# Kernel tuning notes

Measured on AMD Instinct MI355X. Metric: run time of the kernel, lower is better.

The kernel has to match this reference:

```python
import jax, jax.numpy as jnp
import numpy as np

HIDDEN = 768
N_HEADS = 12
HEAD_DIM = HIDDEN // N_HEADS  # 64 (multihead=True)
NEG_BIG = -1e31


def setup_inputs() -> dict:
    key = jax.random.key(0)
    ks = jax.random.split(key, 8)
    B, S = 4, 2048
    toks = jax.random.normal(ks[0], (B, S, HIDDEN), dtype=jnp.float32)
    masks = jax.random.randint(ks[1], (B, S), 0, 2, dtype=jnp.int32)
    s = 0.02
    Wq = jax.random.normal(ks[2], (HIDDEN, HIDDEN), dtype=jnp.float32) * s
    Wk = jax.random.normal(ks[3], (HIDDEN, HIDDEN), dtype=jnp.float32) * s
    Wv = jax.random.normal(ks[4], (HIDDEN, HIDDEN), dtype=jnp.float32) * s
    bq = jax.random.normal(ks[5], (HIDDEN,), dtype=jnp.float32) * s
    bk = jax.random.normal(ks[6], (HIDDEN,), dtype=jnp.float32) * s
    bv = jax.random.normal(ks[7], (HIDDEN,), dtype=jnp.float32) * s
    return {"toks": toks, "masks": masks, "Wq": Wq, "bq": bq,
            "Wk": Wk, "bk": bk, "Wv": Wv, "bv": bv}


def reference(toks, masks, Wq, bq, Wk, bk, Wv, bv):
    B, S, D = toks.shape
    m = masks.astype(jnp.float32)  # [B,S]
    # additive outer-product padding mask: (1 - m_i*m_j) * -1e31, shape [B,S,S]
    add_mask = (1.0 - m[:, :, None] * m[:, None, :]) * NEG_BIG

    def split_heads(x):  # [B,S,D] -> [B,H,S,hd]
        return x.reshape(B, S, N_HEADS, HEAD_DIM).transpose(0, 2, 1, 3)

    q = split_heads(toks @ Wq + bq)
    k = split_heads(toks @ Wk + bk)
    v = split_heads(toks @ Wv + bv)

    scores = jnp.einsum("bhqd,bhkd->bhqk", q, k) / jnp.sqrt(
        jnp.asarray(HEAD_DIM, dtype=toks.dtype))
    scores = scores + add_mask[:, None, :, :]
    probs = jax.nn.softmax(scores, axis=-1)  # dropout is identity at eval
    ctx = jnp.einsum("bhqk,bhkd->bhqd", probs, v)
    return ctx.transpose(0, 2, 1, 3).reshape(B, S, D)
```

## Files before the change

kernel.cpp:

```cpp
#include <hip/hip_runtime.h>
#include <hip/hip_bf16.h>
#include <cstddef>


typedef __bf16 bf16_8 __attribute__((ext_vector_type(8)));
typedef float f32x4 __attribute__((ext_vector_type(4)));
typedef short s16x4 __attribute__((ext_vector_type(4)));
typedef short s16x8 __attribute__((ext_vector_type(8)));

#define HID 768
#define NHEADS 12
#define HD 64
#define BATCH 4
#define SEQ 2048
#define NEGBIG2 (-1.44269504e31f)
#define SCALE2 0.18033688f

#define KT 64
#define NKT (SEQ / KT)
#define STR 68
#define ASTR 40

static __device__ __forceinline__ f32x4 mfma16x16x32(bf16_8 a, bf16_8 b, f32x4 c) {
  return __builtin_amdgcn_mfma_f32_16x16x32_bf16(a, b, c, 0, 0, 0);
}

static __device__ __forceinline__ void lds_barrier() {
  __asm__ volatile("s_waitcnt lgkmcnt(0)\n\ts_barrier" ::: "memory");
}

static __device__ __forceinline__ float fast_exp2(float x) {
#if __has_builtin(__builtin_amdgcn_exp2f)
  return __builtin_amdgcn_exp2f(x);
#else
  return __expf(x * 0.69314718f);
#endif
}

static __device__ __forceinline__ s16x4 pack_bf16x4(f32x4 p) {
  s16x4 o;
#pragma unroll
  for (int i = 0; i < 4; ++i) {
    __bf16 b = (__bf16)p[i];
    o[i] = __builtin_bit_cast(short, b);
  }
  return o;
}

static __device__ __forceinline__ bf16_8 cat2(const __bf16* p) {
  s16x4 lo = *(const s16x4*)p;
  s16x4 hi = *(const s16x4*)(p + 4);
  s16x8 v = __builtin_shufflevector(lo, hi, 0, 1, 2, 3, 4, 5, 6, 7);
  return __builtin_bit_cast(bf16_8, v);
}

static __device__ __forceinline__ void write2(__bf16* p, s16x8 v) {
  *(s16x4*)p = __builtin_shufflevector(v, v, 0, 1, 2, 3);
  *(s16x4*)(p + 4) = __builtin_shufflevector(v, v, 4, 5, 6, 7);
}

static __device__ __forceinline__ bf16_8 cvt_a_frag(const float* p) {
  f32x4 af0 = *(const f32x4*)p;
  f32x4 af1 = *(const f32x4*)(p + 4);
  bf16_8 a;
  a[0] = (__bf16)af0[0]; a[1] = (__bf16)af0[1];
  a[2] = (__bf16)af0[2]; a[3] = (__bf16)af0[3];
  a[4] = (__bf16)af1[0]; a[5] = (__bf16)af1[1];
  a[6] = (__bf16)af1[2]; a[7] = (__bf16)af1[3];
  return a;
}

__global__ __launch_bounds__(256) void mask_kadd(const int* __restrict__ masks,
                                                 float* __restrict__ kaddG) {
  int i = blockIdx.x * 256 + threadIdx.x;
  kaddG[i] = masks[i] ? 0.0f : NEGBIG2;
}

__global__ __launch_bounds__(256) void transpose768x3(const float* __restrict__ Wq,
                                                      const float* __restrict__ Wk,
                                                      const float* __restrict__ Wv,
                                                      __bf16* __restrict__ WtBase) {
  const float* in = blockIdx.z == 0 ? Wq : (blockIdx.z == 1 ? Wk : Wv);
  __bf16* out = WtBase + (size_t)blockIdx.z * HID * HID;
  __shared__ __bf16 tile[32][33];
  int bx = blockIdx.x * 32, by = blockIdx.y * 32;
  int tx = threadIdx.x, ty = threadIdx.y;
#pragma unroll
  for (int r = 0; r < 32; r += 8)
    tile[ty + r][tx] = (__bf16)in[(size_t)(by + ty + r) * HID + bx + tx];
  __syncthreads();
#pragma unroll
  for (int r = 0; r < 32; r += 8)
    out[(size_t)(bx + ty + r) * HID + by + tx] = tile[tx][ty + r];
}

__global__ __launch_bounds__(256, 4) void proj_kv(const float* __restrict__ toks,
                                                  const __bf16* __restrict__ WtK,
                                                  const float* __restrict__ bk,
                                                  const __bf16* __restrict__ WtV,
                                                  const float* __restrict__ bv,
                                                  __bf16* __restrict__ Kout,
                                                  __bf16* __restrict__ Vtout,
                                                  int head0, int hm) {
  __shared__ __align__(16) __bf16 ldsA[2][64 * ASTR];
  int tid = threadIdx.x;
  int w = tid >> 6, lane = tid & 63, l16 = lane & 15, quad = lane >> 4;
  int m0 = blockIdx.x * 64;
  int hl = blockIdx.y, h = head0 + hl;
  int srow = tid >> 2, scg = tid & 3;
  const float* asrc = toks + (size_t)(m0 + srow) * HID + scg * 8;
  const __bf16* bKrow = WtK + (size_t)(h * 64 + w * 16 + l16) * HID + quad * 8;
  const __bf16* bVrow = WtV + (size_t)(h * 64 + w * 16 + l16) * HID + quad * 8;
  f32x4 zero = {0.f, 0.f, 0.f, 0.f};
  f32x4 aK[4], aV[4];
#pragma unroll
  for (int mt = 0; mt < 4; ++mt) { aK[mt] = zero; aV[mt] = zero; }

  *(bf16_8*)(&ldsA[0][srow * ASTR + scg * 8]) = cvt_a_frag(asrc);
  __syncthreads();

  const int NCH = HID / 32;
  for (int t = 0; t < NCH; ++t) {
    int b = t & 1;
    int kk = t * 32;
    bf16_8 areg;
    if (t + 1 < NCH) areg = cvt_a_frag(asrc + kk + 32);
    bf16_8 bkf = *(const bf16_8*)(bKrow + kk);
    bf16_8 bvf = *(const bf16_8*)(bVrow + kk);
#pragma unroll
    for (int mt = 0; mt < 4; ++mt) {
      bf16_8 af = *(const bf16_8*)(&ldsA[b][(mt * 16 + l16) * ASTR + quad * 8]);
      aK[mt] = mfma16x16x32(af, bkf, aK[mt]);
      aV[mt] = mfma16x16x32(af, bvf, aV[mt]);
    }
    if (t + 1 < NCH) {
      *(bf16_8*)(&ldsA[b ^ 1][srow * ASTR + scg * 8]) = areg;
      lds_barrier();
    }
  }

  int d = w * 16 + l16;
  float bnK = bk[h * 64 + d];
  float bnV = bv[h * 64 + d];
#pragma unroll
  for (int mt = 0; mt < 4; ++mt) {
#pragma unroll
    for (int r = 0; r < 4; ++r) {
      int m = m0 + mt * 16 + quad * 4 + r;
      int b = m >> 11;
      int s = m & (SEQ - 1);
      Kout[(((size_t)b * hm + hl) * SEQ + s) * HD + d] = (__bf16)(aK[mt][r] + bnK);
      Vtout[(((size_t)b * hm + hl) * HD + d) * SEQ + s] = (__bf16)(aV[mt][r] + bnV);
    }
  }
}

__global__ __launch_bounds__(256, 3) void attn_fused(const float* __restrict__ toks,
                                                     const __bf16* __restrict__ WtQ,
                                                     const float* __restrict__ bq,
                                                     const __bf16* __restrict__ Kbuf,
                                                     const __bf16* __restrict__ Vtbuf,
                                                     const float* __restrict__ kaddG,
                                                     float* __restrict__ out,
                                                     int head0, int hm) {
  __shared__ __align__(16) __bf16 ldsK[2][64 * STR];
  __shared__ __align__(16) __bf16 ldsV[2][64 * STR];
  __shared__ __align__(16) __bf16 ldsQP[64 * STR];
  int tid = threadIdx.x;
  int w = tid >> 6, lane = tid & 63, l16 = lane & 15, quad = lane >> 4;

  int nwg = gridDim.x * gridDim.y * gridDim.z;
  int hwf = blockIdx.x + gridDim.x * (blockIdx.y + gridDim.y * blockIdx.z);
  int lg = (hwf & 7) * (nwg >> 3) + (hwf >> 3);
  int q0 = (lg & (gridDim.x - 1)) * 64;
  int grp = lg / gridDim.x;
  int hl = grp % hm, bz = grp / hm;
  int h = head0 + hl;

  const float* kb = kaddG + (size_t)bz * SEQ;
  f32x4 zero = {0.f, 0.f, 0.f, 0.f};

  const __bf16* Kb = Kbuf + ((size_t)bz * hm + hl) * SEQ * HD;
  const __bf16* Vb = Vtbuf + ((size_t)bz * hm + hl) * HD * SEQ;

  {
    const float* arow = toks + ((size_t)bz * SEQ + q0 + w * 16 + l16) * HID + quad * 8;
    const __bf16* brow = WtQ + (size_t)(h * 64 + l16) * HID + quad * 8;
    f32x4 qa[4] = {zero, zero, zero, zero};
    for (int kk = 0; kk < HID; kk += 32) {
      bf16_8 a = cvt_a_frag(arow + kk);
#pragma unroll
      for (int t = 0; t < 4; ++t)
        qa[t] = mfma16x16x32(a, *(const bf16_8*)(brow + (size_t)t * 16 * HID + kk), qa[t]);
    }
#pragma unroll
    for (int t = 0; t < 4; ++t) {
      float bn = bq[h * 64 + t * 16 + l16];
#pragma unroll
      for (int r = 0; r < 4; ++r)
        ldsQP[(w * 16 + quad * 4 + r) * STR + t * 16 + l16] = (__bf16)(qa[t][r] + bn);
    }
  }

  int srow = tid >> 3, sc = tid & 7;
  {
    s16x8 k0 = *(const s16x8*)(Kb + (size_t)srow * HD + sc * 8);
    s16x8 k1 = *(const s16x8*)(Kb + (size_t)(srow + 32) * HD + sc * 8);
    s16x8 v0 = *(const s16x8*)(Vb + (size_t)srow * SEQ + sc * 8);
    s16x8 v1 = *(const s16x8*)(Vb + (size_t)(srow + 32) * SEQ + sc * 8);
    write2(&ldsK[0][srow * STR + sc * 8], k0);
    write2(&ldsK[0][(srow + 32) * STR + sc * 8], k1);
    write2(&ldsV[0][srow * STR + sc * 8], v0);
    write2(&ldsV[0][(srow + 32) * STR + sc * 8], v1);
  }
  __syncthreads();

  bf16_8 qf[4][2];
#pragma unroll
  for (int s = 0; s < 4; ++s)
#pragma unroll
    for (int half = 0; half < 2; ++half)
      qf[s][half] = cat2(&ldsQP[(s * 16 + l16) * STR + half * 32 + quad * 8]);
  float actq[4];
#pragma unroll
  for (int s = 0; s < 4; ++s) actq[s] = (kb[q0 + s * 16 + l16] == 0.0f) ? 1.0f : 0.0f;
  __syncthreads();

  float lsum[4] = {0.f, 0.f, 0.f, 0.f};
  f32x4 acc[4];
#pragma unroll
  for (int s = 0; s < 4; ++s) acc[s] = zero;

  for (int t = 0; t < NKT; ++t) {
    int j0 = t * KT;
    int jn = (t + 1 < NKT) ? j0 + KT : 0;
    int buf = t & 1, nbuf = buf ^ 1;
    s16x8 k0 = *(const s16x8*)(Kb + (size_t)(jn + srow) * HD + sc * 8);
    s16x8 k1 = *(const s16x8*)(Kb + (size_t)(jn + srow + 32) * HD + sc * 8);
    s16x8 v0 = *(const s16x8*)(Vb + (size_t)srow * SEQ + jn + sc * 8);
    s16x8 v1 = *(const s16x8*)(Vb + (size_t)(srow + 32) * SEQ + jn + sc * 8);

    bf16_8 kf0 = cat2(&ldsK[buf][(w * 16 + l16) * STR + quad * 8]);
    bf16_8 kf1 = cat2(&ldsK[buf][(w * 16 + l16) * STR + 32 + quad * 8]);
    f32x4 ck = *(const f32x4*)(kb + j0 + w * 16 + quad * 4);
#pragma unroll
    for (int s = 0; s < 4; ++s) {
      f32x4 st = mfma16x16x32(kf1, qf[s][1], mfma16x16x32(kf0, qf[s][0], zero));
      f32x4 p;
#pragma unroll
      for (int r = 0; r < 4; ++r) {
        float v = actq[s] * fmaf(st[r], SCALE2, ck[r]);
        p[r] = fast_exp2(v);
      }
      lsum[s] += p[0] + p[1] + p[2] + p[3];
      *(s16x4*)(&ldsQP[(s * 16 + l16) * STR + w * 16 + quad * 4]) = pack_bf16x4(p);
    }
    lds_barrier();

#pragma unroll
    for (int kc = 0; kc < 2; ++kc) {
      bf16_8 vf = cat2(&ldsV[buf][(w * 16 + l16) * STR + kc * 32 + quad * 8]);
#pragma unroll
      for (int s = 0; s < 4; ++s) {
        bf16_8 pf = cat2(&ldsQP[(s * 16 + l16) * STR + kc * 32 + quad * 8]);
        acc[s] = mfma16x16x32(pf, vf, acc[s]);
      }
    }
    write2(&ldsK[nbuf][srow * STR + sc * 8], k0);
    write2(&ldsK[nbuf][(srow + 32) * STR + sc * 8], k1);
    write2(&ldsV[nbuf][srow * STR + sc * 8], v0);
    write2(&ldsV[nbuf][(srow + 32) * STR + sc * 8], v1);
    lds_barrier();
  }

  __syncthreads();
  float* ls = (float*)ldsQP;
#pragma unroll
  for (int s = 0; s < 4; ++s) {
    float v = lsum[s];
    v += __shfl_xor(v, 16);
    v += __shfl_xor(v, 32);
    if (quad == 0) ls[(w * 4 + s) * 16 + l16] = v;
  }
  __syncthreads();
  float lr[4][4];
#pragma unroll
  for (int s = 0; s < 4; ++s) {
    float tot = ls[(0 * 4 + s) * 16 + l16] + ls[(1 * 4 + s) * 16 + l16] +
                ls[(2 * 4 + s) * 16 + l16] + ls[(3 * 4 + s) * 16 + l16];
    float linv = 1.0f / tot;
#pragma unroll
    for (int r = 0; r < 4; ++r) lr[s][r] = __shfl(linv, quad * 4 + r);
  }
#pragma unroll
  for (int s = 0; s < 4; ++s)
#pragma unroll
    for (int r = 0; r < 4; ++r)
      out[((size_t)bz * SEQ + q0 + s * 16 + quad * 4 + r) * HID + h * HD + w * 16 + l16] =
          acc[s][r] * lr[s][r];
}

extern "C" void kernel_launch(void* const* d_in, const int* in_sizes, int n_in,
                              void* d_out, int out_size, void* d_ws, size_t ws_size,
                              hipStream_t stream) {
  (void)in_sizes; (void)n_in; (void)out_size;
  const float* toks = (const float*)d_in[0];
  const int* masks = (const int*)d_in[1];
  const float* Wq = (const float*)d_in[2];
  const float* bq = (const float*)d_in[3];
  const float* Wk = (const float*)d_in[4];
  const float* bk = (const float*)d_in[5];
  const float* Wv = (const float*)d_in[6];
  const float* bv = (const float*)d_in[7];
  char* ws = (char*)d_ws;
  const size_t KADD_B = (size_t)BATCH * SEQ * 4;
  const size_t WT_B = (size_t)HID * HID * 2;
  const size_t KV_FULL_B = (size_t)BATCH * NHEADS * SEQ * HD * 2;
  const size_t KV_HEAD_B = (size_t)BATCH * SEQ * HD * 2;
  const size_t TIER_A_NEED = KADD_B + 3 * WT_B + 2 * KV_FULL_B;
  float* kaddG = (float*)(ws);
  __bf16* WtQ = (__bf16*)(ws + KADD_B + 0 * WT_B);
  __bf16* WtK = (__bf16*)(ws + KADD_B + 1 * WT_B);
  __bf16* WtV = (__bf16*)(ws + KADD_B + 2 * WT_B);
  float* outp = (float*)d_out;

  mask_kadd<<<BATCH * SEQ / 256, 256, 0, stream>>>(masks, kaddG);
  dim3 tgrid(HID / 32, HID / 32, 3), tblk(32, 8);
  transpose768x3<<<tgrid, tblk, 0, stream>>>(Wq, Wk, Wv, WtQ);

  if (ws_size >= TIER_A_NEED) {
    __bf16* Kf = (__bf16*)(ws + KADD_B + 3 * WT_B);
    __bf16* Vtf = (__bf16*)(ws + KADD_B + 3 * WT_B + KV_FULL_B);
    dim3 pgrid(BATCH * SEQ / 64, NHEADS);
    proj_kv<<<pgrid, 256, 0, stream>>>(toks, WtK, bk, WtV, bv, Kf, Vtf, 0, NHEADS);
    dim3 agrid(SEQ / 64, NHEADS, BATCH);
    attn_fused<<<agrid, 256, 0, stream>>>(toks, WtQ, bq, Kf, Vtf, kaddG, outp, 0, NHEADS);
  } else {
    __bf16* Kh = (__bf16*)(ws + KADD_B + 3 * WT_B);
    __bf16* Vth = (__bf16*)(ws + KADD_B + 3 * WT_B + KV_HEAD_B);
    dim3 pgrid(BATCH * SEQ / 64, 1);
    dim3 agrid(SEQ / 64, 1, BATCH);
    for (int h = 0; h < NHEADS; ++h) {
      proj_kv<<<pgrid, 256, 0, stream>>>(toks, WtK, bk, WtV, bv, Kh, Vth, h, 1);
      attn_fused<<<agrid, 256, 0, stream>>>(toks, WtQ, bq, Kh, Vth, kaddG, outp, h, 1);
    }
  }
}
```

Measured before the change: 304.7 us.

## Give each wave its own query rows to drop mid-loop barrier; prefetch two tiles ahead

Each wave now owns 16 query rows and computes scores against all 64 keys of the tile, so the P matrix stays in a per-wave LDS region. The barrier between softmax and PV becomes a local lgkmcnt wait, and the cross-wave row-sum reduction at the end goes away. K/V global loads are issued two tiles ahead with the loop unrolled by two, giving each load more time to land. The cost is more LDS reads of K and V fragments per wave and more registers held for prefetched tiles.

```diff
diff --git a/kernel.cpp b/kernel.cpp
--- a/kernel.cpp
+++ b/kernel.cpp
@@ -27,6 +27,10 @@
 
 static __device__ __forceinline__ void lds_barrier() {
   __asm__ volatile("s_waitcnt lgkmcnt(0)\n\ts_barrier" ::: "memory");
+}
+
+static __device__ __forceinline__ void lds_flush() {
+  __asm__ volatile("s_waitcnt lgkmcnt(0)" ::: "memory");
 }
 
 static __device__ __forceinline__ float fast_exp2(float x) {
@@ -182,6 +186,7 @@
 
   const __bf16* Kb = Kbuf + ((size_t)bz * hm + hl) * SEQ * HD;
   const __bf16* Vb = Vtbuf + ((size_t)bz * hm + hl) * HD * SEQ;
+  __bf16* Pw = &ldsQP[(w * 16) * STR];
 
   {
     const float* arow = toks + ((size_t)bz * SEQ + q0 + w * 16 + l16) * HID + quad * 8;
@@ -198,9 +203,16 @@
       float bn = bq[h * 64 + t * 16 + l16];
 #pragma unroll
       for (int r = 0; r < 4; ++r)
-        ldsQP[(w * 16 + quad * 4 + r) * STR + t * 16 + l16] = (__bf16)(qa[t][r] + bn);
-    }
-  }
+        Pw[(quad * 4 + r) * STR + t * 16 + l16] = (__bf16)(qa[t][r] + bn);
+    }
+  }
+  lds_flush();
+
+  bf16_8 qf[2];
+#pragma unroll
+  for (int half = 0; half < 2; ++half)
+    qf[half] = cat2(&Pw[l16 * STR + half * 32 + quad * 8]);
+  float actq = (kb[q0 + w * 16 + l16] == 0.0f) ? 1.0f : 0.0f;
 
   int srow = tid >> 3, sc = tid & 7;
   {
@@ -213,91 +225,89 @@
     write2(&ldsV[0][srow * STR + sc * 8], v0);
     write2(&ldsV[0][(srow + 32) * STR + sc * 8], v1);
   }
-  __syncthreads();
-
-  bf16_8 qf[4][2];
-#pragma unroll
-  for (int s = 0; s < 4; ++s)
-#pragma unroll
-    for (int half = 0; half < 2; ++half)
-      qf[s][half] = cat2(&ldsQP[(s * 16 + l16) * STR + half * 32 + quad * 8]);
-  float actq[4];
-#pragma unroll
-  for (int s = 0; s < 4; ++s) actq[s] = (kb[q0 + s * 16 + l16] == 0.0f) ? 1.0f : 0.0f;
-  __syncthreads();
-
-  float lsum[4] = {0.f, 0.f, 0.f, 0.f};
+  s16x8 kA0 = *(const s16x8*)(Kb + (size_t)(KT + srow) * HD + sc * 8);
+  s16x8 kA1 = *(const s16x8*)(Kb + (size_t)(KT + srow + 32) * HD + sc * 8);
+  s16x8 vA0 = *(const s16x8*)(Vb + (size_t)srow * SEQ + KT + sc * 8);
+  s16x8 vA1 = *(const s16x8*)(Vb + (size_t)(srow + 32) * SEQ + KT + sc * 8);
+  s16x8 kB0, kB1, vB0, vB1;
+  lds_barrier();
+
+  float lsum = 0.f;
   f32x4 acc[4];
 #pragma unroll
-  for (int s = 0; s < 4; ++s) acc[s] = zero;
-
-  for (int t = 0; t < NKT; ++t) {
+  for (int dt = 0; dt < 4; ++dt) acc[dt] = zero;
+
+  auto body = [&](int buf, int t) __attribute__((always_inline)) {
     int j0 = t * KT;
-    int jn = (t + 1 < NKT) ? j0 + KT : 0;
-    int buf = t & 1, nbuf = buf ^ 1;
-    s16x8 k0 = *(const s16x8*)(Kb + (size_t)(jn + srow) * HD + sc * 8);
-    s16x8 k1 = *(const s16x8*)(Kb + (size_t)(jn + srow + 32) * HD + sc * 8);
-    s16x8 v0 = *(const s16x8*)(Vb + (size_t)srow * SEQ + jn + sc * 8);
-    s16x8 v1 = *(const s16x8*)(Vb + (size_t)(srow + 32) * SEQ + jn + sc * 8);
-
-    bf16_8 kf0 = cat2(&ldsK[buf][(w * 16 + l16) * STR + quad * 8]);
-    bf16_8 kf1 = cat2(&ldsK[buf][(w * 16 + l16) * STR + 32 + quad * 8]);
-    f32x4 ck = *(const f32x4*)(kb + j0 + w * 16 + quad * 4);
-#pragma unroll
-    for (int s = 0; s < 4; ++s) {
-      f32x4 st = mfma16x16x32(kf1, qf[s][1], mfma16x16x32(kf0, qf[s][0], zero));
+#pragma unroll
+    for (int kbk = 0; kbk < 4; ++kbk) {
+      bf16_8 kf0 = cat2(&ldsK[buf][(kbk * 16 + l16) * STR + quad * 8]);
+      bf16_8 kf1 = cat2(&ldsK[buf][(kbk * 16 + l16) * STR + 32 + quad * 8]);
+      f32x4 st = mfma16x16x32(kf1, qf[1], mfma16x16x32(kf0, qf[0], zero));
+      f32x4 ck = *(const f32x4*)(kb + j0 + kbk * 16 + quad * 4);
       f32x4 p;
 #pragma unroll
       for (int r = 0; r < 4; ++r) {
-        float v = actq[s] * fmaf(st[r], SCALE2, ck[r]);
+        float v = actq * fmaf(st[r], SCALE2, ck[r]);
         p[r] = fast_exp2(v);
       }
-      lsum[s] += p[0] + p[1] + p[2] + p[3];
-      *(s16x4*)(&ldsQP[(s * 16 + l16) * STR + w * 16 + quad * 4]) = pack_bf16x4(p);
-    }
+      lsum += p[0] + p[1] + p[2] + p[3];
+      *(s16x4*)(&Pw[l16 * STR + kbk * 16 + quad * 4]) = pack_bf16x4(p);
+    }
+    lds_flush();
+#pragma unroll
+    for (int kc = 0; kc < 2; ++kc) {
+      bf16_8 pf = cat2(&Pw[l16 * STR + kc * 32 + quad * 8]);
+#pragma unroll
+      for (int dt = 0; dt < 4; ++dt) {
+        bf16_8 vf = cat2(&ldsV[buf][(dt * 16 + l16) * STR + kc * 32 + quad * 8]);
+        acc[dt] = mfma16x16x32(pf, vf, acc[dt]);
+      }
+    }
+  };
+
+  for (int t = 0; t < NKT; t += 2) {
+    {
+      int j2 = (t + 2 < NKT) ? (t + 2) * KT : 0;
+      kB0 = *(const s16x8*)(Kb + (size_t)(j2 + srow) * HD + sc * 8);
+      kB1 = *(const s16x8*)(Kb + (size_t)(j2 + srow + 32) * HD + sc * 8);
+      vB0 = *(const s16x8*)(Vb + (size_t)srow * SEQ + j2 + sc * 8);
+      vB1 = *(const s16x8*)(Vb + (size_t)(srow + 32) * SEQ + j2 + sc * 8);
+    }
+    body(0, t);
+    write2(&ldsK[1][srow * STR + sc * 8], kA0);
+    write2(&ldsK[1][(srow + 32) * STR + sc * 8], kA1);
+    write2(&ldsV[1][srow * STR + sc * 8], vA0);
+    write2(&ldsV[1][(srow + 32) * STR + sc * 8], vA1);
     lds_barrier();
-
-#pragma unroll
-    for (int kc = 0; kc < 2; ++kc) {
-      bf16_8 vf = cat2(&ldsV[buf][(w * 16 + l16) * STR + kc * 32 + quad * 8]);
-#pragma unroll
-      for (int s = 0; s < 4; ++s) {
-        bf16_8 pf = cat2(&ldsQP[(s * 16 + l16) * STR + kc * 32 + quad * 8]);
-        acc[s] = mfma16x16x32(pf, vf, acc[s]);
-      }
-    }
-    write2(&ldsK[nbuf][srow * STR + sc * 8], k0);
-    write2(&ldsK[nbuf][(srow + 32) * STR + sc * 8], k1);
-    write2(&ldsV[nbuf][srow * STR + sc * 8], v0);
-    write2(&ldsV[nbuf][(srow + 32) * STR + sc * 8], v1);
+    {
+      int j3 = (t + 3 < NKT) ? (t + 3) * KT : 0;
+      kA0 = *(const s16x8*)(Kb + (size_t)(j3 + srow) * HD + sc * 8);
+      kA1 = *(const s16x8*)(Kb + (size_t)(j3 + srow + 32) * HD + sc * 8);
+      vA0 = *(const s16x8*)(Vb + (size_t)srow * SEQ + j3 + sc * 8);
+      vA1 = *(const s16x8*)(Vb + (size_t)(srow + 32) * SEQ + j3 + sc * 8);
+    }
+    body(1, t + 1);
+    write2(&ldsK[0][srow * STR + sc * 8], kB0);
+    write2(&ldsK[0][(srow + 32) * STR + sc * 8], kB1);
+    write2(&ldsV[0][srow * STR + sc * 8], vB0);
+    write2(&ldsV[0][(srow + 32) * STR + sc * 8], vB1);
     lds_barrier();
   }
 
-  __syncthreads();
-  float* ls = (float*)ldsQP;
-#pragma unroll
-  for (int s = 0; s < 4; ++s) {
-    float v = lsum[s];
-    v += __shfl_xor(v, 16);
-    v += __shfl_xor(v, 32);
-    if (quad == 0) ls[(w * 4 + s) * 16 + l16] = v;
-  }
-  __syncthreads();
-  float lr[4][4];
-#pragma unroll
-  for (int s = 0; s < 4; ++s) {
-    float tot = ls[(0 * 4 + s) * 16 + l16] + ls[(1 * 4 + s) * 16 + l16] +
-                ls[(2 * 4 + s) * 16 + l16] + ls[(3 * 4 + s) * 16 + l16];
-    float linv = 1.0f / tot;
-#pragma unroll
-    for (int r = 0; r < 4; ++r) lr[s][r] = __shfl(linv, quad * 4 + r);
-  }
-#pragma unroll
-  for (int s = 0; s < 4; ++s)
+  float v = lsum;
+  v += __shfl_xor(v, 16);
+  v += __shfl_xor(v, 32);
+  float linv = 1.0f / v;
+  float lr[4];
+#pragma unroll
+  for (int r = 0; r < 4; ++r) lr[r] = __shfl(linv, quad * 4 + r);
+#pragma unroll
+  for (int dt = 0; dt < 4; ++dt)
 #pragma unroll
     for (int r = 0; r < 4; ++r)
-      out[((size_t)bz * SEQ + q0 + s * 16 + quad * 4 + r) * HID + h * HD + w * 16 + l16] =
-          acc[s][r] * lr[s][r];
+      out[((size_t)bz * SEQ + q0 + w * 16 + quad * 4 + r) * HID + h * HD + dt * 16 + l16] =
+          acc[dt][r] * lr[r];
 }
 
 extern "C" void kernel_launch(void* const* d_in, const int* in_sizes, int n_in,
```

After: 308.9 us. About the same (+1.4%).
